# Optimization experiments

Hardware: AMD Instinct MI355X
Metric: run time of the kernel (lower is better)

The kernel has to match this reference:

```python
import jax, jax.numpy as jnp
import numpy as np

N_NODES = 50000
N_EDGES = 1600000
L = 16  # lifted_dim

def setup_inputs() -> dict:
    key = jax.random.key(0)
    ks = jax.random.split(key, 12)
    M1 = 2 * L          # 32
    M2 = 4 * M1 + 2 * L  # 160
    s = lambda f: 1.0 / np.sqrt(f)
    return {
        "x_s": jax.random.normal(ks[0], (N_NODES, L), jnp.float32),
        "x_t": jax.random.normal(ks[1], (N_NODES, L), jnp.float32),
        "edge_attr": jax.random.normal(ks[2], (N_EDGES, L), jnp.float32),
        "u": jax.random.normal(ks[3], (1, L), jnp.float32),
        "W1a": jax.random.normal(ks[4], (M1, M1), jnp.float32) * s(M1),
        "b1a": jnp.zeros((M1,), jnp.float32),
        "W2a": jax.random.normal(ks[5], (M1, M1), jnp.float32) * s(M1),
        "b2a": jnp.zeros((M1,), jnp.float32),
        "W1b": jax.random.normal(ks[6], (M2, M2), jnp.float32) * s(M2),
        "b1b": jnp.zeros((M2,), jnp.float32),
        "W2b": jax.random.normal(ks[7], (M2, L), jnp.float32) * s(M2),
        "b2b": jnp.zeros((L,), jnp.float32),
        "gamma": jnp.ones((L,), jnp.float32),
        "beta": jnp.zeros((L,), jnp.float32),
        "edge_index": jax.random.randint(ks[8], (2, N_EDGES), 0, N_NODES, jnp.int32),
    }

def _leaky(x, slope):
    return jnp.where(x >= 0, x, slope * x)

def _forward(x_s, x_t, edge_attr, u, W1a, b1a, W2a, b2a, W1b, b1b, W2b, b2b, gamma, beta, edge_index):
    src, tgt = edge_index[0], edge_index[1]
    n = x_s.shape[0]
    # message MLP on gathered neighbor features
    in_msg = jnp.concatenate([x_t[tgt], edge_attr], axis=1)          # [E, 2L]
    h = _leaky(in_msg @ W1a + b1a, 0.1)
    msg = h @ W2a + b2a                                              # [E, 2L]
    # multi-moment segment reduce
    seg = lambda v: jax.ops.segment_sum(v, src, num_segments=n)
    cnt = seg(jnp.ones((msg.shape[0], 1), msg.dtype))
    denom = jnp.maximum(cnt, 1.0)
    mean = seg(msg) / denom                                          # [N, 2L]
    var = _leaky(seg(msg * msg) / denom - mean * mean, 0.01)
    std = jnp.sqrt(var + 1e-6)
    z = (msg - mean[src]) / std[src]                                 # standardized per-edge
    skew = jnp.nan_to_num(seg(z ** 3) / denom, nan=0.0)
    kurt = jnp.nan_to_num(seg(z ** 4) / denom, nan=0.0)
    h_cat = jnp.concatenate([x_s, mean, std, skew, kurt,
                             jnp.broadcast_to(u, (n, u.shape[1]))], axis=-1)  # [N, 10L]
    h2 = _leaky(h_cat @ W1b + b1b, 0.1)
    out = h2 @ W2b + b2b                                             # [N, L]
    # BatchNorm1d (training-mode batch stats, eps=1e-5)
    mu = jnp.mean(out, axis=0)
    vb = jnp.mean((out - mu) ** 2, axis=0)
    return gamma * (out - mu) * jax.lax.rsqrt(vb + 1e-5) + beta

def reference(x_s, x_t, edge_attr, u, W1a, b1a, W2a, b2a, W1b, b1b, W2b, b2b, gamma, beta, edge_index):
    return _forward(x_s, x_t, edge_attr, u, W1a, b1a, W2a, b2a, W1b, b1b, W2b, b2b, gamma, beta, edge_index)
```

## Files before the change

kernel.cpp:

```cpp
#include <hip/hip_runtime.h>

#define N_NODES 50000
#define N_EDGES 1600000

#define EPB 8192
#define NB1 ((N_EDGES + EPB - 1) / EPB)
#define NPB 128
#define NBK ((N_NODES + NPB - 1) / NPB)
#define TBL (NBK * NB1)
#define NSB ((TBL + 255) / 256)
#define MAXB 4608
#define SCATB 1024
#define NFT 512
#define SUBP 2048
#define NSUB (EPB / SUBP)

typedef unsigned short ushort_t;
typedef __attribute__((ext_vector_type(8))) __bf16 bf16x8;
typedef __attribute__((ext_vector_type(4))) float  f32x4;

union FU { ushort_t s[8]; bf16x8 v; };

__device__ __forceinline__ ushort_t f2bf(float f) {
    union { float f; unsigned int i; } v; v.f = f;
    unsigned int r = v.i + 0x7fffu + ((v.i >> 16) & 1u);
    return (ushort_t)(r >> 16);
}
__device__ __forceinline__ float leaky(float x, float s) { return x >= 0.f ? x : s * x; }

__global__ __launch_bounds__(SCATB) void k_bcount(const int* __restrict__ src, int* __restrict__ table,
                                                  const float* __restrict__ x_t, ushort_t* __restrict__ x_tb) {
    __shared__ int cnt[NBK];
    const int t = threadIdx.x, blk = blockIdx.x;
    const int g = blk * SCATB + t;
    if (g < (N_NODES * 16) / 4) {
        f32x4 v = ((const f32x4*)x_t)[g];
        unsigned long long p = (unsigned long long)f2bf(v[0])
                             | ((unsigned long long)f2bf(v[1]) << 16)
                             | ((unsigned long long)f2bf(v[2]) << 32)
                             | ((unsigned long long)f2bf(v[3]) << 48);
        ((unsigned long long*)x_tb)[g] = p;
    }
    for (int i = t; i < NBK; i += SCATB) cnt[i] = 0;
    __syncthreads();
    const int base = blk * EPB;
    for (int i = t; i < EPB; i += SCATB) {
        int e = base + i;
        if (e < N_EDGES) atomicAdd(&cnt[src[e] >> 7], 1);
    }
    __syncthreads();
    for (int b = t; b < NBK; b += SCATB) table[b * NB1 + blk] = cnt[b];
}

__global__ __launch_bounds__(256) void k_scan1(int* __restrict__ table, int* __restrict__ bsum) {
    __shared__ int buf[256];
    const int t = threadIdx.x, i = blockIdx.x * 256 + t;
    int v = (i < TBL) ? table[i] : 0;
    buf[t] = v; __syncthreads();
    for (int off = 1; off < 256; off <<= 1) {
        int x = (t >= off) ? buf[t - off] : 0;
        __syncthreads(); buf[t] += x; __syncthreads();
    }
    int incl = buf[t];
    if (i < TBL) table[i] = incl - v;
    if (t == 255) bsum[blockIdx.x] = incl;
}
__global__ __launch_bounds__(256) void k_scan2(int* __restrict__ bsum, float* __restrict__ bnsum) {
    __shared__ int sums[256];
    const int t = threadIdx.x;
    if (t < 32) bnsum[t] = 0.f;
    const int SEG = (NSB + 255) / 256;
    const int s0 = t * SEG, s1 = (s0 + SEG < NSB) ? s0 + SEG : NSB;
    int sum = 0;
    for (int i = s0; i < s1; i++) sum += bsum[i];
    sums[t] = sum; __syncthreads();
    for (int off = 1; off < 256; off <<= 1) {
        int x = (t >= off) ? sums[t - off] : 0;
        __syncthreads(); sums[t] += x; __syncthreads();
    }
    int carry = sums[t] - sum;
    for (int i = s0; i < s1; i++) { int v = bsum[i]; bsum[i] = carry; carry += v; }
}

__global__ __launch_bounds__(SCATB) void k_bscat(const int* __restrict__ src, const int* __restrict__ tgt,
                                                 const float* __restrict__ ea, const int* __restrict__ table,
                                                 const int* __restrict__ bsum,
                                                 int* __restrict__ tnA, ushort_t* __restrict__ eaA) {
    __shared__ int curG[NBK];
    __shared__ int cntL[NBK];
    __shared__ int curL[NBK];
    __shared__ int scanS[512];
    __shared__ ushort_t bucketL[SUBP];
    __shared__ __align__(16) ushort_t recbuf[SUBP * 16];

    const int t = threadIdx.x, blk = blockIdx.x;
    for (int i = t; i < NBK; i += SCATB) {
        int idx = i * NB1 + blk;
        curG[i] = table[idx] + bsum[idx >> 8];
        cntL[i] = 0; curL[i] = 0;
    }
    __syncthreads();
    const int cbase = blk * EPB;

    for (int sp = 0; sp < NSUB; sp++) {
        const int sbase = cbase + sp * SUBP;
        const int m = (N_EDGES - sbase < SUBP) ? (N_EDGES - sbase) : SUBP;

        for (int i = t; i < m; i += SCATB) atomicAdd(&cntL[src[sbase + i] >> 7], 1);
        __syncthreads();
        if (t < 512) scanS[t] = (t < NBK) ? cntL[t] : 0;
        __syncthreads();
        for (int off = 1; off < 512; off <<= 1) {
            int x = (t < 512 && t >= off) ? scanS[t - off] : 0;
            __syncthreads();
            if (t < 512) scanS[t] += x;
            __syncthreads();
        }
        if (t < NBK) scanS[t] -= cntL[t];
        __syncthreads();
        for (int i = t; i < m; i += SCATB) {
            int e = sbase + i;
            int s = src[e];
            int b = s >> 7;
            int loc = scanS[b] + atomicAdd(&curL[b], 1);
            bucketL[loc] = (ushort_t)b;
            int gpos = curG[b] + (loc - scanS[b]);
            tnA[gpos] = tgt[e] | ((s & (NPB - 1)) << 16);
            const f32x4* ep = (const f32x4*)(ea + (size_t)e * 16);
            f32x4 v0 = __builtin_nontemporal_load(ep);
            f32x4 v1 = __builtin_nontemporal_load(ep + 1);
            f32x4 v2 = __builtin_nontemporal_load(ep + 2);
            f32x4 v3 = __builtin_nontemporal_load(ep + 3);
            FU lo, hi;
            #pragma unroll
            for (int j = 0; j < 4; j++) {
                lo.s[j] = f2bf(v0[j]); lo.s[4 + j] = f2bf(v1[j]);
                hi.s[j] = f2bf(v2[j]); hi.s[4 + j] = f2bf(v3[j]);
            }
            *(bf16x8*)(recbuf + loc * 16)     = lo.v;
            *(bf16x8*)(recbuf + loc * 16 + 8) = hi.v;
        }
        __syncthreads();
        for (int loc = t; loc < m; loc += SCATB) {
            int b = bucketL[loc];
            int gpos = curG[b] + (loc - scanS[b]);
            bf16x8 lo = *(bf16x8*)(recbuf + loc * 16);
            bf16x8 hi = *(bf16x8*)(recbuf + loc * 16 + 8);
            *(bf16x8*)(eaA + (size_t)gpos * 16)     = lo;
            *(bf16x8*)(eaA + (size_t)gpos * 16 + 8) = hi;
        }
        __syncthreads();
        for (int i = t; i < NBK; i += SCATB) {
            curG[i] += cntL[i];
            cntL[i] = 0; curL[i] = 0;
        }
        __syncthreads();
    }
}

__global__ __launch_bounds__(NFT) void k_nodeF(
    const ushort_t* __restrict__ x_tb, const ushort_t* __restrict__ eaA, const int* __restrict__ tnA,
    const int* __restrict__ table, const int* __restrict__ bsum,
    const float* __restrict__ w1a, const float* __restrict__ b1a,
    const float* __restrict__ w2a, const float* __restrict__ b2a,
    const float* __restrict__ x_s, const float* __restrict__ u,
    ushort_t* __restrict__ hcat)
{
    __shared__ ushort_t permL[MAXB];
    __shared__ ushort_t tgL[MAXB];
    __shared__ int cntL[NPB], scanL[NPB], curL[NPB];
    __shared__ __align__(16) float h_lds[8][16][36];
    __shared__ ushort_t stat_lds[8][128];

    const int t = threadIdx.x;
    const int w = t >> 6, L = t & 63, q = L >> 4, c = L & 15;
    const int b = blockIdx.x;
    const int i0   = b * NB1;
    const int base = table[i0] + bsum[i0 >> 8];
    int end;
    if (b < NBK - 1) { const int i1 = (b + 1) * NB1; end = table[i1] + bsum[i1 >> 8]; }
    else end = N_EDGES;
    const int cntB0 = end - base;
    const int cntB  = cntB0 < MAXB ? cntB0 : MAXB;

    if (t < NPB) cntL[t] = 0;
    __syncthreads();
    for (int i = t; i < cntB; i += NFT) {
        int v = tnA[base + i];
        tgL[i] = (ushort_t)(v & 0xFFFF);
        atomicAdd(&cntL[v >> 16], 1);
    }
    __syncthreads();
    if (t == 0) {
        int s = 0;
        for (int nl = 0; nl < NPB; nl++) { scanL[nl] = s; s += cntL[nl]; }
    }
    __syncthreads();
    if (t < NPB) curL[t] = scanL[t];
    __syncthreads();
    for (int i = t; i < cntB; i += NFT) {
        int nl = tnA[base + i] >> 16;
        int loc = atomicAdd(&curL[nl], 1);
        permL[loc] = (ushort_t)i;
    }

    bf16x8 B1[2], B2[2];
    #pragma unroll
    for (int h = 0; h < 2; h++) {
        FU u1, u2;
        #pragma unroll
        for (int j = 0; j < 8; j++) {
            int kk = q * 8 + j, nn = c + 16 * h;
            u1.s[j] = f2bf(w1a[kk * 32 + nn]);
            u2.s[j] = f2bf(w2a[kk * 32 + nn]);
        }
        B1[h] = u1.v; B2[h] = u2.v;
    }
    const float bias1[2] = { b1a[c], b1a[c + 16] };
    const float bias2[2] = { b2a[c], b2a[c + 16] };
    const f32x4 zero = { 0.f, 0.f, 0.f, 0.f };
    __syncthreads();

    for (int kn = 0; kn < 16; kn++) {
        const int nl = w * 16 + kn;
        const int n  = b * NPB + nl;
        const int startL = scanL[nl], d = cntL[nl];
        float s1a = 0.f, s2a = 0.f, s3a = 0.f, s4a = 0.f;
        float s1b = 0.f, s2b = 0.f, s3b = 0.f, s4b = 0.f;
        const int ntl = (d + 15) >> 4;

        for (int tl = 0; tl < ntl; tl++) {
            int row  = tl * 16 + c;
            int ridx = row < d ? row : d - 1;
            int li   = permL[startL + ridx];
            FU af;
            if (q < 2) {
                int tg = tgL[li];
                __builtin_memcpy(&af.v, x_tb + (size_t)tg * 16 + q * 8, 16);
            } else {
                __builtin_memcpy(&af.v, eaA + (size_t)(base + li) * 16 + (q - 2) * 8, 16);
            }

            f32x4 a0 = __builtin_amdgcn_mfma_f32_16x16x32_bf16(af.v, B1[0], zero, 0, 0, 0);
            f32x4 a1 = __builtin_amdgcn_mfma_f32_16x16x32_bf16(af.v, B1[1], zero, 0, 0, 0);
            #pragma unroll
            for (int r = 0; r < 4; r++) {
                h_lds[w][q * 4 + r][c]      = leaky(a0[r] + bias1[0], 0.1f);
                h_lds[w][q * 4 + r][c + 16] = leaky(a1[r] + bias1[1], 0.1f);
            }
            __asm__ volatile("s_waitcnt lgkmcnt(0)" ::: "memory");

            float hv[8];
            __builtin_memcpy(&hv, &h_lds[w][c][q * 8], 32);
            FU hf;
            #pragma unroll
            for (int j = 0; j < 8; j++) hf.s[j] = f2bf(hv[j]);
            f32x4 m0 = __builtin_amdgcn_mfma_f32_16x16x32_bf16(hf.v, B2[0], zero, 0, 0, 0);
            f32x4 m1 = __builtin_amdgcn_mfma_f32_16x16x32_bf16(hf.v, B2[1], zero, 0, 0, 0);

            int rb = tl * 16 + q * 4;
            #pragma unroll
            for (int r = 0; r < 4; r++) {
                if (rb + r < d) {
                    float m = m0[r] + bias2[0], mm = m * m;
                    s1a += m;  s2a += mm; s3a += mm * m; s4a += mm * mm;
                    float x = m1[r] + bias2[1], xx = x * x;
                    s1b += x;  s2b += xx; s3b += xx * x; s4b += xx * xx;
                }
            }
        }

        if (n >= N_NODES) continue;

        s1a += __shfl_xor(s1a, 16); s1a += __shfl_xor(s1a, 32);
        s2a += __shfl_xor(s2a, 16); s2a += __shfl_xor(s2a, 32);
        s3a += __shfl_xor(s3a, 16); s3a += __shfl_xor(s3a, 32);
        s4a += __shfl_xor(s4a, 16); s4a += __shfl_xor(s4a, 32);
        s1b += __shfl_xor(s1b, 16); s1b += __shfl_xor(s1b, 32);
        s2b += __shfl_xor(s2b, 16); s2b += __shfl_xor(s2b, 32);
        s3b += __shfl_xor(s3b, 16); s3b += __shfl_xor(s3b, 32);
        s4b += __shfl_xor(s4b, 16); s4b += __shfl_xor(s4b, 32);

        if (q == 0) {
            float denom = fmaxf((float)d, 1.f);
            {
                float mean = s1a / denom, m2r = s2a / denom, m3r = s3a / denom, m4r = s4a / denom;
                float var  = leaky(m2r - mean * mean, 0.01f);
                float stdv = sqrtf(var + 1e-6f);
                float e3   = m3r - 3.f * mean * m2r + 2.f * mean * mean * mean;
                float skew = e3 / (stdv * stdv * stdv);
                float e4   = m4r - 4.f * mean * m3r + 6.f * mean * mean * m2r
                             - 3.f * mean * mean * mean * mean;
                float kurt = e4 / (stdv * stdv * stdv * stdv);
                stat_lds[w][c]      = f2bf(mean);
                stat_lds[w][32 + c] = f2bf(stdv);
                stat_lds[w][64 + c] = f2bf(skew);
                stat_lds[w][96 + c] = f2bf(kurt);
            }
            {
                float mean = s1b / denom, m2r = s2b / denom, m3r = s3b / denom, m4r = s4b / denom;
                float var  = leaky(m2r - mean * mean, 0.01f);
                float stdv = sqrtf(var + 1e-6f);
                float e3   = m3r - 3.f * mean * m2r + 2.f * mean * mean * mean;
                float skew = e3 / (stdv * stdv * stdv);
                float e4   = m4r - 4.f * mean * m3r + 6.f * mean * mean * m2r
                             - 3.f * mean * mean * mean * mean;
                float kurt = e4 / (stdv * stdv * stdv * stdv);
                stat_lds[w][16 + c]  = f2bf(mean);
                stat_lds[w][48 + c]  = f2bf(stdv);
                stat_lds[w][80 + c]  = f2bf(skew);
                stat_lds[w][112 + c] = f2bf(kurt);
            }
        }
        __asm__ volatile("s_waitcnt lgkmcnt(0)" ::: "memory");

        const size_t basep = (size_t)n * 160;
        unsigned int sv;
        __builtin_memcpy(&sv, &stat_lds[w][L * 2], 4);
        *(unsigned int*)(hcat + basep + 16 + L * 2) = sv;
        if (L < 16) {
            hcat[basep + L]       = f2bf(x_s[(size_t)n * 16 + L]);
            hcat[basep + 144 + L] = f2bf(u[L]);
        }
    }
}

__global__ __launch_bounds__(256) void k_gemm1(const ushort_t* __restrict__ hcat,
                                               const float* __restrict__ w1b,
                                               const float* __restrict__ b1b,
                                               ushort_t* __restrict__ h2)
{
    __shared__ __align__(16) ushort_t W1T[160 * 168];
    int t = threadIdx.x;
    for (int i = t; i < 160 * 160; i += 256) { int k = i / 160, n = i % 160; W1T[n * 168 + k] = f2bf(w1b[i]); }
    __syncthreads();
    int w = t >> 6, L = t & 63, q = L >> 4, c = L & 15;
    const f32x4 zero = { 0.f, 0.f, 0.f, 0.f };
    for (int tile = blockIdx.x * 4 + w; tile < 3125 * 10; tile += gridDim.x * 4) {
        int rt = tile / 10, nt = tile % 10;
        int m = rt * 16 + c, n = nt * 16 + c;
        f32x4 acc = zero;
        #pragma unroll
        for (int ks = 0; ks < 5; ks++) {
            bf16x8 a; __builtin_memcpy(&a, hcat + (size_t)m * 160 + ks * 32 + q * 8, 16);
            bf16x8 b; __builtin_memcpy(&b, &W1T[n * 168 + ks * 32 + q * 8], 16);
            acc = __builtin_amdgcn_mfma_f32_16x16x32_bf16(a, b, acc, 0, 0, 0);
        }
        float bias = b1b[n];
        #pragma unroll
        for (int r = 0; r < 4; r++) {
            h2[(size_t)(rt * 16 + q * 4 + r) * 160 + n] = f2bf(leaky(acc[r] + bias, 0.1f));
        }
    }
}

__global__ __launch_bounds__(256) void k_gemm2(const ushort_t* __restrict__ h2,
                                               const float* __restrict__ w2b,
                                               const float* __restrict__ b2b,
                                               float* __restrict__ outpre, float* __restrict__ bnsum)
{
    __shared__ __align__(16) ushort_t W2T[16 * 168];
    int t = threadIdx.x;
    for (int i = t; i < 160 * 16; i += 256) { int k = i / 16, n = i % 16; W2T[n * 168 + k] = f2bf(w2b[i]); }
    __syncthreads();
    int w = t >> 6, L = t & 63, q = L >> 4, c = L & 15;
    const f32x4 zero = { 0.f, 0.f, 0.f, 0.f };
    float ps = 0.f, ps2 = 0.f;
    float bias = b2b[c];
    for (int rt = blockIdx.x * 4 + w; rt < 3125; rt += gridDim.x * 4) {
        int m = rt * 16 + c;
        f32x4 acc = zero;
        #pragma unroll
        for (int ks = 0; ks < 5; ks++) {
            bf16x8 a; __builtin_memcpy(&a, h2 + (size_t)m * 160 + ks * 32 + q * 8, 16);
            bf16x8 b; __builtin_memcpy(&b, &W2T[c * 168 + ks * 32 + q * 8], 16);
            acc = __builtin_amdgcn_mfma_f32_16x16x32_bf16(a, b, acc, 0, 0, 0);
        }
        #pragma unroll
        for (int r = 0; r < 4; r++) {
            float v = acc[r] + bias;
            outpre[(size_t)(rt * 16 + q * 4 + r) * 16 + c] = v;
            ps += v; ps2 += v * v;
        }
    }
    ps  += __shfl_xor(ps, 16);  ps  += __shfl_xor(ps, 32);
    ps2 += __shfl_xor(ps2, 16); ps2 += __shfl_xor(ps2, 32);
    if (q == 0) {
        unsafeAtomicAdd(&bnsum[c], ps);
        unsafeAtomicAdd(&bnsum[16 + c], ps2);
    }
}

__global__ __launch_bounds__(256) void k_bn(const float* __restrict__ outpre, const float* __restrict__ bnsum,
                                            const float* __restrict__ gamma, const float* __restrict__ beta,
                                            float* __restrict__ out)
{
    int i = blockIdx.x * 256 + threadIdx.x;
    int c = i & 15;
    float x = outpre[i];
    float mu = bnsum[c] * (1.f / N_NODES);
    float var = bnsum[16 + c] * (1.f / N_NODES) - mu * mu;
    out[i] = gamma[c] * (x - mu) * rsqrtf(var + 1e-5f) + beta[c];
}

extern "C" void kernel_launch(void* const* d_in, const int* in_sizes, int n_in,
                              void* d_out, int out_size, void* d_ws, size_t ws_size,
                              hipStream_t stream) {
    const float* x_s  = (const float*)d_in[0];
    const float* x_t  = (const float*)d_in[1];
    const float* ea   = (const float*)d_in[2];
    const float* u    = (const float*)d_in[3];
    const float* w1a  = (const float*)d_in[4];
    const float* b1a  = (const float*)d_in[5];
    const float* w2a  = (const float*)d_in[6];
    const float* b2a  = (const float*)d_in[7];
    const float* w1b  = (const float*)d_in[8];
    const float* b1b  = (const float*)d_in[9];
    const float* w2b  = (const float*)d_in[10];
    const float* b2b  = (const float*)d_in[11];
    const float* gam  = (const float*)d_in[12];
    const float* bet  = (const float*)d_in[13];
    const int* eidx   = (const int*)d_in[14];
    const int* src = eidx;
    const int* tgt = eidx + N_EDGES;

    char* ws = (char*)d_ws;
    const size_t OFF_TABLE  = 0;
    const size_t OFF_BSUM   = 614400;
    const size_t OFF_BNSUM  = 655360;
    const size_t OFF_OUTPRE = 786432;
    const size_t OFF_XTB    = 4194304;
    const size_t OFF_TNA    = 6291456;
    const size_t OFF_EAA    = 16777216;
    const size_t OFF_HCAT   = 68157440;
    const size_t OFF_H2     = 84934656;

    int*      table  = (int*)(ws + OFF_TABLE);
    int*      bsum   = (int*)(ws + OFF_BSUM);
    float*    bnsum  = (float*)(ws + OFF_BNSUM);
    float*    outpre = (float*)(ws + OFF_OUTPRE);
    ushort_t* x_tb   = (ushort_t*)(ws + OFF_XTB);
    int*      tnA    = (int*)(ws + OFF_TNA);
    ushort_t* eaA    = (ushort_t*)(ws + OFF_EAA);
    ushort_t* hcat   = (ushort_t*)(ws + OFF_HCAT);
    ushort_t* h2     = (ushort_t*)(ws + OFF_H2);

    k_bcount<<<NB1, SCATB, 0, stream>>>(src, table, x_t, x_tb);
    k_scan1 <<<NSB, 256, 0, stream>>>(table, bsum);
    k_scan2 <<<1,   256, 0, stream>>>(bsum, bnsum);
    k_bscat <<<NB1, SCATB, 0, stream>>>(src, tgt, ea, table, bsum, tnA, eaA);
    k_nodeF <<<NBK, NFT, 0, stream>>>(x_tb, eaA, tnA, table, bsum, w1a, b1a, w2a, b2a, x_s, u, hcat);
    k_gemm1 <<<1024, 256, 0, stream>>>(hcat, w1b, b1b, h2);
    k_gemm2 <<<512,  256, 0, stream>>>(h2, w2b, b2b, outpre, bnsum);
    k_bn    <<<(N_NODES * 16) / 256, 256, 0, stream>>>(outpre, bnsum, gam, bet, (float*)d_out);
}
```

Baseline: 404.2 us.

## Use packed bf16 convert, double nodeF block size, store target ids in sorted order

Replaces the software round-to-nearest bf16 conversion with the hardware v_cvt_pk_bf16_f32 instruction in several kernels. It also doubles k_nodeF's thread count to 1024 so each wave handles 8 nodes instead of 16, and grows the per-wave LDS arrays to match. Target ids are now written in permuted order, which removes one indirect LDS lookup on the x_t gather path. The larger block raises LDS use per block and may limit how many blocks fit per CU. The hardware convert may also round NaN or other edge cases differently from the software version.

After: 392.3 us. -2.9%, faster.

```diff
diff --git a/kernel.cpp b/kernel.cpp
--- a/kernel.cpp
+++ b/kernel.cpp
@@ -11,7 +11,7 @@
 #define NSB ((TBL + 255) / 256)
 #define MAXB 4608
 #define SCATB 1024
-#define NFT 512
+#define NFT 1024
 #define SUBP 2048
 #define NSUB (EPB / SUBP)
 
@@ -19,12 +19,17 @@
 typedef __attribute__((ext_vector_type(8))) __bf16 bf16x8;
 typedef __attribute__((ext_vector_type(4))) float  f32x4;
 
-union FU { ushort_t s[8]; bf16x8 v; };
+union FU { ushort_t s[8]; unsigned int u[4]; bf16x8 v; };
 
 __device__ __forceinline__ ushort_t f2bf(float f) {
     union { float f; unsigned int i; } v; v.f = f;
     unsigned int r = v.i + 0x7fffu + ((v.i >> 16) & 1u);
     return (ushort_t)(r >> 16);
+}
+__device__ __forceinline__ unsigned int cvtpk(float lo, float hi) {
+    unsigned int r;
+    asm("v_cvt_pk_bf16_f32 %0, %1, %2" : "=v"(r) : "v"(lo), "v"(hi));
+    return r;
 }
 __device__ __forceinline__ float leaky(float x, float s) { return x >= 0.f ? x : s * x; }
 
@@ -35,10 +40,8 @@
     const int g = blk * SCATB + t;
     if (g < (N_NODES * 16) / 4) {
         f32x4 v = ((const f32x4*)x_t)[g];
-        unsigned long long p = (unsigned long long)f2bf(v[0])
-                             | ((unsigned long long)f2bf(v[1]) << 16)
-                             | ((unsigned long long)f2bf(v[2]) << 32)
-                             | ((unsigned long long)f2bf(v[3]) << 48);
+        unsigned long long p = (unsigned long long)cvtpk(v[0], v[1])
+                             | ((unsigned long long)cvtpk(v[2], v[3]) << 32);
         ((unsigned long long*)x_tb)[g] = p;
     }
     for (int i = t; i < NBK; i += SCATB) cnt[i] = 0;
@@ -132,11 +135,10 @@
             f32x4 v2 = __builtin_nontemporal_load(ep + 2);
             f32x4 v3 = __builtin_nontemporal_load(ep + 3);
             FU lo, hi;
-            #pragma unroll
-            for (int j = 0; j < 4; j++) {
-                lo.s[j] = f2bf(v0[j]); lo.s[4 + j] = f2bf(v1[j]);
-                hi.s[j] = f2bf(v2[j]); hi.s[4 + j] = f2bf(v3[j]);
-            }
+            lo.u[0] = cvtpk(v0[0], v0[1]); lo.u[1] = cvtpk(v0[2], v0[3]);
+            lo.u[2] = cvtpk(v1[0], v1[1]); lo.u[3] = cvtpk(v1[2], v1[3]);
+            hi.u[0] = cvtpk(v2[0], v2[1]); hi.u[1] = cvtpk(v2[2], v2[3]);
+            hi.u[2] = cvtpk(v3[0], v3[1]); hi.u[3] = cvtpk(v3[2], v3[3]);
             *(bf16x8*)(recbuf + loc * 16)     = lo.v;
             *(bf16x8*)(recbuf + loc * 16 + 8) = hi.v;
         }
@@ -167,10 +169,10 @@
     ushort_t* __restrict__ hcat)
 {
     __shared__ ushort_t permL[MAXB];
-    __shared__ ushort_t tgL[MAXB];
+    __shared__ ushort_t tgC[MAXB];
     __shared__ int cntL[NPB], scanL[NPB], curL[NPB];
-    __shared__ __align__(16) float h_lds[8][16][36];
-    __shared__ ushort_t stat_lds[8][128];
+    __shared__ __align__(16) float h_lds[16][16][36];
+    __shared__ ushort_t stat_lds[16][128];
 
     const int t = threadIdx.x;
     const int w = t >> 6, L = t & 63, q = L >> 4, c = L & 15;
@@ -185,11 +187,8 @@
 
     if (t < NPB) cntL[t] = 0;
     __syncthreads();
-    for (int i = t; i < cntB; i += NFT) {
-        int v = tnA[base + i];
-        tgL[i] = (ushort_t)(v & 0xFFFF);
-        atomicAdd(&cntL[v >> 16], 1);
-    }
+    for (int i = t; i < cntB; i += NFT)
+        atomicAdd(&cntL[tnA[base + i] >> 16], 1);
     __syncthreads();
     if (t == 0) {
         int s = 0;
@@ -199,9 +198,10 @@
     if (t < NPB) curL[t] = scanL[t];
     __syncthreads();
     for (int i = t; i < cntB; i += NFT) {
-        int nl = tnA[base + i] >> 16;
-        int loc = atomicAdd(&curL[nl], 1);
+        int v = tnA[base + i];
+        int loc = atomicAdd(&curL[v >> 16], 1);
         permL[loc] = (ushort_t)i;
+        tgC[loc]   = (ushort_t)(v & 0xFFFF);
     }
 
     bf16x8 B1[2], B2[2];
@@ -221,8 +221,8 @@
     const f32x4 zero = { 0.f, 0.f, 0.f, 0.f };
     __syncthreads();
 
-    for (int kn = 0; kn < 16; kn++) {
-        const int nl = w * 16 + kn;
+    for (int kn = 0; kn < 8; kn++) {
+        const int nl = w * 8 + kn;
         const int n  = b * NPB + nl;
         const int startL = scanL[nl], d = cntL[nl];
         float s1a = 0.f, s2a = 0.f, s3a = 0.f, s4a = 0.f;
@@ -232,12 +232,13 @@
         for (int tl = 0; tl < ntl; tl++) {
             int row  = tl * 16 + c;
             int ridx = row < d ? row : d - 1;
-            int li   = permL[startL + ridx];
+            int pidx = startL + ridx;
             FU af;
             if (q < 2) {
-                int tg = tgL[li];
+                int tg = tgC[pidx];
                 __builtin_memcpy(&af.v, x_tb + (size_t)tg * 16 + q * 8, 16);
             } else {
+                int li = permL[pidx];
                 __builtin_memcpy(&af.v, eaA + (size_t)(base + li) * 16 + (q - 2) * 8, 16);
             }
 
@@ -253,8 +254,8 @@
             float hv[8];
             __builtin_memcpy(&hv, &h_lds[w][c][q * 8], 32);
             FU hf;
-            #pragma unroll
-            for (int j = 0; j < 8; j++) hf.s[j] = f2bf(hv[j]);
+            hf.u[0] = cvtpk(hv[0], hv[1]); hf.u[1] = cvtpk(hv[2], hv[3]);
+            hf.u[2] = cvtpk(hv[4], hv[5]); hf.u[3] = cvtpk(hv[6], hv[7]);
             f32x4 m0 = __builtin_amdgcn_mfma_f32_16x16x32_bf16(hf.v, B2[0], zero, 0, 0, 0);
             f32x4 m1 = __builtin_amdgcn_mfma_f32_16x16x32_bf16(hf.v, B2[1], zero, 0, 0, 0);
 
```
